# Kernel tuning notes

Hardware: AMD Instinct MI355X
Metric: run time of the kernel (lower is better)

The kernel has to match this reference:

```python
import jax, jax.numpy as jnp
import numpy as np

B, S, D = 4, 4096, 128

def setup_inputs() -> dict:
    key = jax.random.key(0)
    kq, kk, kv = jax.random.split(key, 3)
    q = jax.random.normal(kq, (B, S, D), dtype=jnp.float32)
    k = jax.random.normal(kk, (B, S, D), dtype=jnp.float32)
    v = jax.random.normal(kv, (B, S, D), dtype=jnp.float32)
    return {"q": q, "k": k, "v": v}

def reference(q, k, v):
    d_model = q.shape[-1]
    scale = 1.0 / jnp.sqrt(jnp.asarray(d_model, q.dtype))
    # [B, S, S] scores
    scores = jnp.einsum('bqd,bkd->bqk', q, k) * scale
    s = q.shape[1]
    causal = jnp.tril(jnp.ones((s, s), dtype=bool))
    neg_inf = jnp.asarray(-jnp.inf, scores.dtype)
    scores = jnp.where(causal[None, :, :], scores, neg_inf)
    attn = jax.nn.softmax(scores, axis=-1)
    return jnp.einsum('bqk,bkd->bqd', attn, v)
```

## Files before the change

kernel.cpp:

```cpp
#include <hip/hip_runtime.h>


#define B_   4
#define S_   4096
#define D_   128
#define BN   64
#define NT_  64
#define QT_  32
#define RMAX 4
#define BLOB_SHORTS 16384
#define MASKVAL (-1.0e30f)

typedef __attribute__((ext_vector_type(8))) short bf16x8;
typedef __attribute__((ext_vector_type(4))) float f32x4;
typedef __attribute__((ext_vector_type(16))) float f32x16;

__device__ __forceinline__ short f2bf(float x) {
    unsigned u = __builtin_bit_cast(unsigned, x);
    unsigned r = (u + 0x7fffu + ((u >> 16) & 1u)) >> 16;
    return (short)r;
}
__device__ __forceinline__ float ex2(float x) { return __builtin_amdgcn_exp2f(x); }
__device__ __forceinline__ unsigned pkbf(float lo, float hi) {
    return (unsigned)(unsigned short)f2bf(lo) | ((unsigned)(unsigned short)f2bf(hi) << 16);
}
__device__ __forceinline__ void gl_lds16(const short* g, short* l) {
    __builtin_amdgcn_global_load_lds(
        (const __attribute__((address_space(1))) unsigned int*)g,
        (__attribute__((address_space(3))) unsigned int*)l, 16, 0, 0);
}

__global__ __launch_bounds__(256) void prep(const float* __restrict__ Qg,
                                            const float* __restrict__ Kg,
                                            const float* __restrict__ Vg,
                                            short* __restrict__ Qbf,
                                            short* __restrict__ KV)
{
    __shared__ short vt[64][40];
    const int id  = blockIdx.x;
    const int tid = threadIdx.x;
    const float SC = 0.12751740f;

    if (id < 1024) {
        const int b = id & 3, tile = (id >> 2) & 63, q4 = id >> 8;
        const int n = q4 * 16 + (tid >> 4);
        const int G = tid & 15;
        const size_t rowoff = ((size_t)b * S_ + (size_t)tile * 64 + n) * D_ + G * 8;
        short* blob = KV + (size_t)(b * NT_ + tile) * BLOB_SHORTS;
        {
            float4 a = *reinterpret_cast<const float4*>(Qg + rowoff);
            float4 c = *reinterpret_cast<const float4*>(Qg + rowoff + 4);
            bf16x8 v;
            v[0] = f2bf(a.x * SC); v[1] = f2bf(a.y * SC); v[2] = f2bf(a.z * SC); v[3] = f2bf(a.w * SC);
            v[4] = f2bf(c.x * SC); v[5] = f2bf(c.y * SC); v[6] = f2bf(c.z * SC); v[7] = f2bf(c.w * SC);
            *reinterpret_cast<bf16x8*>(Qbf + rowoff) = v;
        }
        {
            float4 a = *reinterpret_cast<const float4*>(Kg + rowoff);
            float4 c = *reinterpret_cast<const float4*>(Kg + rowoff + 4);
            bf16x8 v;
            v[0] = f2bf(a.x); v[1] = f2bf(a.y); v[2] = f2bf(a.z); v[3] = f2bf(a.w);
            v[4] = f2bf(c.x); v[5] = f2bf(c.y); v[6] = f2bf(c.z); v[7] = f2bf(c.w);
            const int p = (G & 8) | ((G & 7) ^ (n & 7));
            *reinterpret_cast<bf16x8*>(blob + n * 128 + p * 8) = v;
        }
    } else {
        const int u = id - 1024;
        const int b = u & 3, tile = (u >> 2) & 63, dq = u >> 8;
        short* blob = KV + (size_t)(b * NT_ + tile) * BLOB_SHORTS;
        {
            const int n = tid >> 2, c8 = tid & 3;
            const size_t off = ((size_t)b * S_ + (size_t)tile * 64 + n) * D_ + dq * 32 + c8 * 8;
            float4 a = *reinterpret_cast<const float4*>(Vg + off);
            float4 c = *reinterpret_cast<const float4*>(Vg + off + 4);
            bf16x8 v;
            v[0] = f2bf(a.x); v[1] = f2bf(a.y); v[2] = f2bf(a.z); v[3] = f2bf(a.w);
            v[4] = f2bf(c.x); v[5] = f2bf(c.y); v[6] = f2bf(c.z); v[7] = f2bf(c.w);
            *reinterpret_cast<bf16x8*>(&vt[n][c8 * 8]) = v;
        }
        __syncthreads();
        {
            const int dl = tid >> 3, G = tid & 7;
            const int d  = dq * 32 + dl;
            bf16x8 g;
#pragma unroll
            for (int i = 0; i < 8; ++i) g[i] = vt[G * 8 + i][dl];
            const int p = G ^ (d & 7);
            *reinterpret_cast<bf16x8*>(blob + 8192 + d * 64 + p * 8) = g;
        }
    }
}

template<bool SPLIT>
__global__ __launch_bounds__(256, 2) void fa_fwd(const short* __restrict__ Qbf,
                                                 const short* __restrict__ KV,
                                                 float* __restrict__ Og,
                                                 float* __restrict__ Op,
                                                 float* __restrict__ Ml,
                                                 int R)
{
    __shared__ short lkv[2][BLOB_SHORTS];

    const int tid  = threadIdx.x;
    const int wv   = tid >> 6;
    const int lane = tid & 63;
    const int col  = lane & 31;
    const int half = lane >> 5;
    const int c7   = col & 7;

    int batch, t, lo, hi, chunk_id;
    {
        const int id = blockIdx.x;
        batch = id & 3;
        if (SPLIT) {
            int u = id >> 2;
            int tt = u / R;
            int r  = u - tt * R;
            t  = QT_ - 1 - tt;
            const int nk = 2 * t + 2;
            lo = r * nk / R;
            hi = (r + 1) * nk / R;
            chunk_id = (batch * QT_ + t) * R + r;
            if (lo >= hi) return;
        } else {
            t  = QT_ - 1 - (id >> 2);
            lo = 0; hi = 2 * t + 2; chunk_id = 0;
        }
    }

    bf16x8 qf[8];
    {
        const short* qp = Qbf + ((size_t)batch * S_ + (size_t)t * 128 + wv * 32 + col) * D_ + half * 8;
#pragma unroll
        for (int c = 0; c < 8; ++c)
            qf[c] = *reinterpret_cast<const bf16x8*>(qp + c * 16);
    }

    f32x16 acc[4];
#pragma unroll
    for (int i = 0; i < 4; ++i)
#pragma unroll
        for (int r = 0; r < 16; ++r) acc[i][r] = 0.f;
    float mrun = MASKVAL, lrun = 0.f;

    const size_t tilebase = (size_t)batch * NT_ * BLOB_SHORTS;
#define STAGE(KT, BUF) do {                                                   \
        const short* g_ = KV + tilebase + (size_t)(KT) * BLOB_SHORTS + tid * 8;\
        short* l_ = (BUF) + tid * 8;                                          \
        _Pragma("unroll")                                                     \
        for (int c_ = 0; c_ < 8; ++c_)                                        \
            gl_lds16(g_ + c_ * 2048, l_ + c_ * 2048);                         \
    } while (0)

    STAGE(lo, lkv[0]);

    for (int kt = lo; kt < hi; ++kt) {
        const short* cur = lkv[(kt - lo) & 1];
        short* nxt = lkv[(kt - lo + 1) & 1];
        __syncthreads();
        if (kt + 1 < hi) STAGE(kt + 1, nxt);

        const short* lk = cur;
        const short* lv = cur + 8192;

        f32x16 st[2];
#pragma unroll
        for (int i = 0; i < 2; ++i)
#pragma unroll
            for (int r = 0; r < 16; ++r) st[i][r] = 0.f;
#pragma unroll
        for (int c = 0; c < 8; ++c) {
            const int G = 2 * c + half;
            const int p = (G & 8) | ((G & 7) ^ c7);
#pragma unroll
            for (int kt32 = 0; kt32 < 2; ++kt32) {
                const int n = kt32 * 32 + col;
                bf16x8 kf = *reinterpret_cast<const bf16x8*>(lk + n * 128 + p * 8);
                st[kt32] = __builtin_amdgcn_mfma_f32_32x32x16_bf16(kf, qf[c], st[kt32], 0, 0, 0);
            }
        }

        if (kt >= 2 * t) {
            const int kbase = (kt - 2 * t) * 64;
            const int qloc  = wv * 32 + col;
#pragma unroll
            for (int kt32 = 0; kt32 < 2; ++kt32)
#pragma unroll
                for (int r = 0; r < 16; ++r) {
                    const int kl = kt32 * 32 + (r & 3) + 8 * (r >> 2) + 4 * half;
                    if (kbase + kl > qloc) st[kt32][r] = MASKVAL;
                }
        }

        float mx = MASKVAL;
#pragma unroll
        for (int i = 0; i < 2; ++i)
#pragma unroll
            for (int r = 0; r < 16; ++r) mx = fmaxf(mx, st[i][r]);
        mx = fmaxf(mx, __shfl_xor(mx, 32));
        const float mnew = fmaxf(mrun, mx);
        const float al   = ex2(mrun - mnew);
        mrun = mnew;
        float sum = 0.f;
#pragma unroll
        for (int i = 0; i < 2; ++i)
#pragma unroll
            for (int r = 0; r < 16; ++r) {
                float pv = ex2(st[i][r] - mnew);
                st[i][r] = pv;
                sum += pv;
            }
        sum += __shfl_xor(sum, 32);
        lrun = lrun * al + sum;
#pragma unroll
        for (int i = 0; i < 4; ++i)
#pragma unroll
            for (int r = 0; r < 16; ++r) acc[i][r] *= al;

#pragma unroll
        for (int kt32 = 0; kt32 < 2; ++kt32) {
            unsigned pw[4][2];
#pragma unroll
            for (int w = 0; w < 4; ++w) {
                pw[w][0] = pkbf(st[kt32][4 * w],     st[kt32][4 * w + 1]);
                pw[w][1] = pkbf(st[kt32][4 * w + 2], st[kt32][4 * w + 3]);
            }
#pragma unroll
            for (int s1 = 0; s1 < 2; ++s1) {
                unsigned snd0 = pw[2 * s1 + 1 - half][0];
                unsigned snd1 = pw[2 * s1 + 1 - half][1];
                unsigned rcv0 = __shfl_xor((int)snd0, 32);
                unsigned rcv1 = __shfl_xor((int)snd1, 32);
                unsigned own0 = pw[2 * s1 + half][0];
                unsigned own1 = pw[2 * s1 + half][1];
                int4 wi;
                wi.x = (int)(half ? rcv0 : own0);
                wi.y = (int)(half ? rcv1 : own1);
                wi.z = (int)(half ? own0 : rcv0);
                wi.w = (int)(half ? own1 : rcv1);
                bf16x8 pf = __builtin_bit_cast(bf16x8, wi);
                const int step = kt32 * 2 + s1;
                const int G = 2 * step + half;
                const int p = G ^ c7;
#pragma unroll
                for (int dt = 0; dt < 4; ++dt) {
                    const int d = dt * 32 + col;
                    bf16x8 vf = *reinterpret_cast<const bf16x8*>(lv + d * 64 + p * 8);
                    acc[dt] = __builtin_amdgcn_mfma_f32_32x32x16_bf16(vf, pf, acc[dt], 0, 0, 0);
                }
            }
        }
    }
#undef STAGE

    const int qloc = wv * 32 + col;
    if (SPLIT) {
        float* ob = Op + (size_t)chunk_id * (128 * D_) + (size_t)qloc * D_;
#pragma unroll
        for (int dt = 0; dt < 4; ++dt)
#pragma unroll
            for (int g = 0; g < 4; ++g) {
                const int d0 = dt * 32 + 8 * g + 4 * half;
                f32x4 v4 = {acc[dt][4 * g], acc[dt][4 * g + 1], acc[dt][4 * g + 2], acc[dt][4 * g + 3]};
                *reinterpret_cast<f32x4*>(ob + d0) = v4;
            }
        if (half == 0) {
            float* mlb = Ml + (size_t)chunk_id * (128 * 2) + qloc * 2;
            mlb[0] = mrun;
            mlb[1] = lrun;
        }
    } else {
        const float inv = 1.0f / lrun;
        float* og = Og + ((size_t)batch * S_ + (size_t)t * 128 + qloc) * D_;
#pragma unroll
        for (int dt = 0; dt < 4; ++dt)
#pragma unroll
            for (int g = 0; g < 4; ++g) {
                const int d0 = dt * 32 + 8 * g + 4 * half;
                f32x4 v4 = {acc[dt][4 * g] * inv, acc[dt][4 * g + 1] * inv,
                            acc[dt][4 * g + 2] * inv, acc[dt][4 * g + 3] * inv};
                *reinterpret_cast<f32x4*>(og + d0) = v4;
            }
    }
}

template<int RR>
__global__ __launch_bounds__(256) void fa_merge(const float* __restrict__ Op,
                                                const float* __restrict__ Ml,
                                                float* __restrict__ Og)
{
    const int x   = blockIdx.x;
    const int btq = x >> 4;
    const int oct = x & 15;
    const int t   = btq & (QT_ - 1);
    const int nk  = 2 * t + 2;
    const int row = oct * 8 + (threadIdx.x >> 5);
    const int cg  = threadIdx.x & 31;
    const size_t cbase = (size_t)btq * RR;

    float mg = MASKVAL;
#pragma unroll
    for (int r = 0; r < RR; ++r) {
        int lo = r * nk / RR, hi = (r + 1) * nk / RR;
        if (lo < hi) mg = fmaxf(mg, Ml[(cbase + r) * (128 * 2) + row * 2]);
    }
    float l = 0.f;
    f32x4 a = (f32x4){0.f, 0.f, 0.f, 0.f};
#pragma unroll
    for (int r = 0; r < RR; ++r) {
        int lo = r * nk / RR, hi = (r + 1) * nk / RR;
        if (lo >= hi) continue;
        float mr = Ml[(cbase + r) * (128 * 2) + row * 2];
        float lr = Ml[(cbase + r) * (128 * 2) + row * 2 + 1];
        float w  = ex2(mr - mg);
        l += lr * w;
        a += w * *reinterpret_cast<const f32x4*>(Op + (cbase + r) * (128 * D_) + row * D_ + cg * 4);
    }
    *reinterpret_cast<f32x4*>(Og + (size_t)btq * (128 * D_) + row * D_ + cg * 4) = a * (1.0f / l);
}

extern "C" void kernel_launch(void* const* d_in, const int* in_sizes, int n_in,
                              void* d_out, int out_size, void* d_ws, size_t ws_size,
                              hipStream_t stream) {
    const float* q = (const float*)d_in[0];
    const float* k = (const float*)d_in[1];
    const float* v = (const float*)d_in[2];
    float* o = (float*)d_out;

    const size_t QBF_BYTES = (size_t)B_ * S_ * D_ * 2;
    const size_t KV_BYTES  = (size_t)B_ * NT_ * BLOB_SHORTS * 2;
    const size_t PREFIX    = QBF_BYTES + KV_BYTES;
    const size_t O_FLOATS  = (size_t)B_ * QT_ * 128 * D_;
    const size_t ML_FLOATS = (size_t)B_ * QT_ * 128 * 2;
    const size_t PER_R     = (O_FLOATS + ML_FLOATS) * sizeof(float);

    char* ws = (char*)d_ws;
    short* Qbf = (short*)ws;
    short* KV  = (short*)(ws + QBF_BYTES);

    int R = 0;
    if (ws_size > PREFIX) {
        R = (int)((ws_size - PREFIX) / PER_R);
        if (R > RMAX) R = RMAX;
    }

    prep<<<dim3(2048), 256, 0, stream>>>(q, k, v, Qbf, KV);

    if (R >= 1) {
        float* Op = (float*)(ws + PREFIX);
        float* Ml = Op + (size_t)R * O_FLOATS;
        fa_fwd<true><<<dim3(B_ * QT_ * R), 256, 0, stream>>>(Qbf, KV, nullptr, Op, Ml, R);
        switch (R) {
            case 1: fa_merge<1><<<dim3(B_ * QT_ * 16), 256, 0, stream>>>(Op, Ml, o); break;
            case 2: fa_merge<2><<<dim3(B_ * QT_ * 16), 256, 0, stream>>>(Op, Ml, o); break;
            case 3: fa_merge<3><<<dim3(B_ * QT_ * 16), 256, 0, stream>>>(Op, Ml, o); break;
            default: fa_merge<4><<<dim3(B_ * QT_ * 16), 256, 0, stream>>>(Op, Ml, o); break;
        }
    } else {
        fa_fwd<false><<<dim3(B_ * QT_), 256, 0, stream>>>(Qbf, KV, o, nullptr, nullptr, 1);
    }
}
```

Baseline: 124.9 us.

## Replace per-tile KV split with perfectly balanced flattened work partition

Flattens all causal (query tile, KV tile) pairs per batch into one linear sequence of 1056 units and gives each of 128 blocks per batch an equal contiguous slice of about 8 units. Blocks that cross query-tile boundaries flush partial outputs and reload Q, so every block does the same amount of work instead of splitting each query tile into a fixed R chunks. Partial outputs are now stored as bf16 to halve merge traffic. This trades extra partial-slot writes and bf16 rounding of partials for even load across CUs, and the merge kernel now reads a variable number of slots per tile.

```diff
diff --git a/kernel.cpp b/kernel.cpp
--- a/kernel.cpp
+++ b/kernel.cpp
@@ -4,10 +4,11 @@
 #define B_   4
 #define S_   4096
 #define D_   128
-#define BN   64
 #define NT_  64
 #define QT_  32
-#define RMAX 4
+#define JB   128
+#define W_   1056
+#define SLOTS_PB 160
 #define BLOB_SHORTS 16384
 #define MASKVAL (-1.0e30f)
 
@@ -24,11 +25,15 @@
 __device__ __forceinline__ unsigned pkbf(float lo, float hi) {
     return (unsigned)(unsigned short)f2bf(lo) | ((unsigned)(unsigned short)f2bf(hi) << 16);
 }
+__device__ __forceinline__ float bf2f(short s) {
+    return __builtin_bit_cast(float, ((unsigned)(unsigned short)s) << 16);
+}
 __device__ __forceinline__ void gl_lds16(const short* g, short* l) {
     __builtin_amdgcn_global_load_lds(
         (const __attribute__((address_space(1))) unsigned int*)g,
         (__attribute__((address_space(3))) unsigned int*)l, 16, 0, 0);
 }
+__device__ __forceinline__ int chunk_of(int v) { return (4 * v + 3) / 33; }
 
 __global__ __launch_bounds__(256) void prep(const float* __restrict__ Qg,
                                             const float* __restrict__ Kg,
@@ -91,13 +96,10 @@
     }
 }
 
-template<bool SPLIT>
-__global__ __launch_bounds__(256, 2) void fa_fwd(const short* __restrict__ Qbf,
+__global__ __launch_bounds__(256, 2) void fa_bal(const short* __restrict__ Qbf,
                                                  const short* __restrict__ KV,
-                                                 float* __restrict__ Og,
-                                                 float* __restrict__ Op,
-                                                 float* __restrict__ Ml,
-                                                 int R)
+                                                 short* __restrict__ Opb,
+                                                 float* __restrict__ Ml)
 {
     __shared__ short lkv[2][BLOB_SHORTS];
 
@@ -108,40 +110,23 @@
     const int half = lane >> 5;
     const int c7   = col & 7;
 
-    int batch, t, lo, hi, chunk_id;
-    {
-        const int id = blockIdx.x;
-        batch = id & 3;
-        if (SPLIT) {
-            int u = id >> 2;
-            int tt = u / R;
-            int r  = u - tt * R;
-            t  = QT_ - 1 - tt;
-            const int nk = 2 * t + 2;
-            lo = r * nk / R;
-            hi = (r + 1) * nk / R;
-            chunk_id = (batch * QT_ + t) * R + r;
-            if (lo >= hi) return;
-        } else {
-            t  = QT_ - 1 - (id >> 2);
-            lo = 0; hi = 2 * t + 2; chunk_id = 0;
-        }
-    }
-
-    bf16x8 qf[8];
-    {
-        const short* qp = Qbf + ((size_t)batch * S_ + (size_t)t * 128 + wv * 32 + col) * D_ + half * 8;
-#pragma unroll
-        for (int c = 0; c < 8; ++c)
-            qf[c] = *reinterpret_cast<const bf16x8*>(qp + c * 16);
-    }
-
-    f32x16 acc[4];
-#pragma unroll
-    for (int i = 0; i < 4; ++i)
-#pragma unroll
-        for (int r = 0; r < 16; ++r) acc[i][r] = 0.f;
-    float mrun = MASKVAL, lrun = 0.f;
+    const int batch = blockIdx.x & 3;
+    const int j     = blockIdx.x >> 2;
+    const int v0    = (33 * j) >> 2;
+    const int v1    = (33 * (j + 1)) >> 2;
+
+    int t = (int)((sqrtf((float)(4 * v0 + 1)) - 1.0f) * 0.5f);
+    while ((t + 1) * (t + 2) <= v0) ++t;
+    while (t * (t + 1) > v0) --t;
+    int ktl = v0 - t * (t + 1);
+
+    int base = 0;
+    for (int tt = 0; tt < t; ++tt) {
+        int a = chunk_of(tt * (tt + 1));
+        int b2 = chunk_of((tt + 1) * (tt + 2) - 1);
+        base += b2 - a + 1;
+    }
+    int slot = batch * SLOTS_PB + base + (j - chunk_of(t * (t + 1)));
 
     const size_t tilebase = (size_t)batch * NT_ * BLOB_SHORTS;
 #define STAGE(KT, BUF) do {                                                   \
@@ -151,14 +136,35 @@
         for (int c_ = 0; c_ < 8; ++c_)                                        \
             gl_lds16(g_ + c_ * 2048, l_ + c_ * 2048);                         \
     } while (0)
-
-    STAGE(lo, lkv[0]);
-
-    for (int kt = lo; kt < hi; ++kt) {
-        const short* cur = lkv[(kt - lo) & 1];
-        short* nxt = lkv[(kt - lo + 1) & 1];
+#define LOADQ(T) do {                                                         \
+        const short* qp_ = Qbf + ((size_t)batch * S_ + (size_t)(T) * 128      \
+                                  + wv * 32 + col) * D_ + half * 8;           \
+        _Pragma("unroll")                                                     \
+        for (int c_ = 0; c_ < 8; ++c_)                                        \
+            qf[c_] = *reinterpret_cast<const bf16x8*>(qp_ + c_ * 16);         \
+    } while (0)
+
+    bf16x8 qf[8];
+    LOADQ(t);
+
+    f32x16 acc[4];
+#pragma unroll
+    for (int i = 0; i < 4; ++i)
+#pragma unroll
+        for (int r = 0; r < 16; ++r) acc[i][r] = 0.f;
+    float mrun = MASKVAL, lrun = 0.f;
+
+    STAGE(ktl, lkv[0]);
+
+    for (int v = v0; v < v1; ++v) {
+        const short* cur = lkv[(v - v0) & 1];
+        short* nxt = lkv[(v - v0 + 1) & 1];
+
+        int nt = t, nktl = ktl + 1;
+        if (nktl == 2 * t + 2) { nt = t + 1; nktl = 0; }
+
         __syncthreads();
-        if (kt + 1 < hi) STAGE(kt + 1, nxt);
+        if (v + 1 < v1) STAGE(nktl, nxt);
 
         const short* lk = cur;
         const short* lv = cur + 8192;
@@ -180,8 +186,8 @@
             }
         }
 
-        if (kt >= 2 * t) {
-            const int kbase = (kt - 2 * t) * 64;
+        if (ktl >= 2 * t) {
+            const int kbase = (ktl - 2 * t) * 64;
             const int qloc  = wv * 32 + col;
 #pragma unroll
             for (int kt32 = 0; kt32 < 2; ++kt32)
@@ -239,8 +245,7 @@
                 wi.z = (int)(half ? own0 : rcv0);
                 wi.w = (int)(half ? own1 : rcv1);
                 bf16x8 pf = __builtin_bit_cast(bf16x8, wi);
-                const int step = kt32 * 2 + s1;
-                const int G = 2 * step + half;
+                const int G = 2 * (kt32 * 2 + s1) + half;
                 const int p = G ^ c7;
 #pragma unroll
                 for (int dt = 0; dt < 4; ++dt) {
@@ -250,73 +255,230 @@
                 }
             }
         }
+
+        if (nktl == 0 || v + 1 == v1) {
+            short* ob = Opb + (size_t)slot * (128 * D_) + tid * 64;
+#pragma unroll
+            for (int dt = 0; dt < 4; ++dt)
+#pragma unroll
+                for (int g = 0; g < 4; ++g) {
+                    int2 w;
+                    w.x = (int)pkbf(acc[dt][4 * g],     acc[dt][4 * g + 1]);
+                    w.y = (int)pkbf(acc[dt][4 * g + 2], acc[dt][4 * g + 3]);
+                    *reinterpret_cast<int2*>(ob + (dt * 4 + g) * 4) = w;
+                }
+            if (half == 0) {
+                float* mlb = Ml + (size_t)slot * (128 * 2) + (wv * 32 + col) * 2;
+                mlb[0] = mrun;
+                mlb[1] = lrun;
+            }
+            if (v + 1 < v1) {
+                int a = chunk_of(t * (t + 1));
+                int b2 = chunk_of((t + 1) * (t + 2) - 1);
+                base += b2 - a + 1;
+                slot = batch * SLOTS_PB + base + (j - chunk_of(nt * (nt + 1)));
+                LOADQ(nt);
+#pragma unroll
+                for (int i = 0; i < 4; ++i)
+#pragma unroll
+                    for (int r = 0; r < 16; ++r) acc[i][r] = 0.f;
+                mrun = MASKVAL; lrun = 0.f;
+            }
+        }
+        t = nt; ktl = nktl;
     }
 #undef STAGE
-
-    const int qloc = wv * 32 + col;
-    if (SPLIT) {
-        float* ob = Op + (size_t)chunk_id * (128 * D_) + (size_t)qloc * D_;
-#pragma unroll
-        for (int dt = 0; dt < 4; ++dt)
-#pragma unroll
-            for (int g = 0; g < 4; ++g) {
-                const int d0 = dt * 32 + 8 * g + 4 * half;
-                f32x4 v4 = {acc[dt][4 * g], acc[dt][4 * g + 1], acc[dt][4 * g + 2], acc[dt][4 * g + 3]};
-                *reinterpret_cast<f32x4*>(ob + d0) = v4;
-            }
-        if (half == 0) {
-            float* mlb = Ml + (size_t)chunk_id * (128 * 2) + qloc * 2;
-            mlb[0] = mrun;
-            mlb[1] = lrun;
-        }
-    } else {
-        const float inv = 1.0f / lrun;
-        float* og = Og + ((size_t)batch * S_ + (size_t)t * 128 + qloc) * D_;
-#pragma unroll
-        for (int dt = 0; dt < 4; ++dt)
-#pragma unroll
-            for (int g = 0; g < 4; ++g) {
-                const int d0 = dt * 32 + 8 * g + 4 * half;
-                f32x4 v4 = {acc[dt][4 * g] * inv, acc[dt][4 * g + 1] * inv,
-                            acc[dt][4 * g + 2] * inv, acc[dt][4 * g + 3] * inv};
-                *reinterpret_cast<f32x4*>(og + d0) = v4;
-            }
-    }
-}
-
-template<int RR>
-__global__ __launch_bounds__(256) void fa_merge(const float* __restrict__ Op,
+#undef LOADQ
+}
+
+__global__ __launch_bounds__(256) void fa_merge(const short* __restrict__ Opb,
                                                 const float* __restrict__ Ml,
                                                 float* __restrict__ Og)
 {
     const int x   = blockIdx.x;
     const int btq = x >> 4;
     const int oct = x & 15;
+    const int b   = btq >> 5;
     const int t   = btq & (QT_ - 1);
-    const int nk  = 2 * t + 2;
-    const int row = oct * 8 + (threadIdx.x >> 5);
+    const int q   = oct * 8 + (threadIdx.x >> 5);
     const int cg  = threadIdx.x & 31;
-    const size_t cbase = (size_t)btq * RR;
+
+    const int jlo = chunk_of(t * (t + 1));
+    const int jhi = chunk_of((t + 1) * (t + 2) - 1);
+    const int cnt = jhi - jlo + 1;
+    int base = 0;
+    for (int tt = 0; tt < t; ++tt) {
+        int a = chunk_of(tt * (tt + 1));
+        int b2 = chunk_of((tt + 1) * (tt + 2) - 1);
+        base += b2 - a + 1;
+    }
+    const int slot0 = b * SLOTS_PB + base;
+
+    const int t_id  = (q >> 5) * 64 + (cg & 1) * 32 + (q & 31);
+    const int inner = (cg >> 3) * 4 + ((cg >> 1) & 3);
+    const int d0    = (cg >> 3) * 32 + ((cg >> 1) & 3) * 8 + (cg & 1) * 4;
 
     float mg = MASKVAL;
-#pragma unroll
-    for (int r = 0; r < RR; ++r) {
-        int lo = r * nk / RR, hi = (r + 1) * nk / RR;
-        if (lo < hi) mg = fmaxf(mg, Ml[(cbase + r) * (128 * 2) + row * 2]);
-    }
+    for (int r = 0; r < cnt; ++r)
+        mg = fmaxf(mg, Ml[(size_t)(slot0 + r) * (128 * 2) + q * 2]);
     float l = 0.f;
     f32x4 a = (f32x4){0.f, 0.f, 0.f, 0.f};
-#pragma unroll
-    for (int r = 0; r < RR; ++r) {
-        int lo = r * nk / RR, hi = (r + 1) * nk / RR;
-        if (lo >= hi) continue;
-        float mr = Ml[(cbase + r) * (128 * 2) + row * 2];
-        float lr = Ml[(cbase + r) * (128 * 2) + row * 2 + 1];
+    for (int r = 0; r < cnt; ++r) {
+        const size_t sl = (size_t)(slot0 + r);
+        float mr = Ml[sl * (128 * 2) + q * 2];
+        float lr = Ml[sl * (128 * 2) + q * 2 + 1];
         float w  = ex2(mr - mg);
         l += lr * w;
-        a += w * *reinterpret_cast<const f32x4*>(Op + (cbase + r) * (128 * D_) + row * D_ + cg * 4);
-    }
-    *reinterpret_cast<f32x4*>(Og + (size_t)btq * (128 * D_) + row * D_ + cg * 4) = a * (1.0f / l);
+        short4 s = *reinterpret_cast<const short4*>(
+            Opb + sl * (128 * D_) + t_id * 64 + inner * 4);
+        a[0] += w * bf2f(s.x);
+        a[1] += w * bf2f(s.y);
+        a[2] += w * bf2f(s.z);
+        a[3] += w * bf2f(s.w);
+    }
+    *reinterpret_cast<f32x4*>(Og + (size_t)btq * (128 * D_) + q * D_ + d0) = a * (1.0f / l);
+}
+
+__global__ __launch_bounds__(256, 2) void fa_direct(const short* __restrict__ Qbf,
+                                                    const short* __restrict__ KV,
+                                                    float* __restrict__ Og)
+{
+    __shared__ short lkv[2][BLOB_SHORTS];
+    const int tid  = threadIdx.x;
+    const int wv   = tid >> 6;
+    const int lane = tid & 63;
+    const int col  = lane & 31;
+    const int half = lane >> 5;
+    const int c7   = col & 7;
+    const int batch = blockIdx.x & 3;
+    const int t     = QT_ - 1 - (blockIdx.x >> 2);
+    const int hi    = 2 * t + 2;
+
+    bf16x8 qf[8];
+    {
+        const short* qp = Qbf + ((size_t)batch * S_ + (size_t)t * 128 + wv * 32 + col) * D_ + half * 8;
+#pragma unroll
+        for (int c = 0; c < 8; ++c) qf[c] = *reinterpret_cast<const bf16x8*>(qp + c * 16);
+    }
+    f32x16 acc[4];
+#pragma unroll
+    for (int i = 0; i < 4; ++i)
+#pragma unroll
+        for (int r = 0; r < 16; ++r) acc[i][r] = 0.f;
+    float mrun = MASKVAL, lrun = 0.f;
+    const size_t tilebase = (size_t)batch * NT_ * BLOB_SHORTS;
+#define STAGE(KT, BUF) do {                                                   \
+        const short* g_ = KV + tilebase + (size_t)(KT) * BLOB_SHORTS + tid * 8;\
+        short* l_ = (BUF) + tid * 8;                                          \
+        _Pragma("unroll")                                                     \
+        for (int c_ = 0; c_ < 8; ++c_)                                        \
+            gl_lds16(g_ + c_ * 2048, l_ + c_ * 2048);                         \
+    } while (0)
+    STAGE(0, lkv[0]);
+    for (int kt = 0; kt < hi; ++kt) {
+        const short* cur = lkv[kt & 1];
+        short* nxt = lkv[(kt + 1) & 1];
+        __syncthreads();
+        if (kt + 1 < hi) STAGE(kt + 1, nxt);
+        const short* lk = cur;
+        const short* lv = cur + 8192;
+        f32x16 st[2];
+#pragma unroll
+        for (int i = 0; i < 2; ++i)
+#pragma unroll
+            for (int r = 0; r < 16; ++r) st[i][r] = 0.f;
+#pragma unroll
+        for (int c = 0; c < 8; ++c) {
+            const int G = 2 * c + half;
+            const int p = (G & 8) | ((G & 7) ^ c7);
+#pragma unroll
+            for (int kt32 = 0; kt32 < 2; ++kt32) {
+                const int n = kt32 * 32 + col;
+                bf16x8 kf = *reinterpret_cast<const bf16x8*>(lk + n * 128 + p * 8);
+                st[kt32] = __builtin_amdgcn_mfma_f32_32x32x16_bf16(kf, qf[c], st[kt32], 0, 0, 0);
+            }
+        }
+        if (kt >= 2 * t) {
+            const int kbase = (kt - 2 * t) * 64;
+            const int qloc  = wv * 32 + col;
+#pragma unroll
+            for (int kt32 = 0; kt32 < 2; ++kt32)
+#pragma unroll
+                for (int r = 0; r < 16; ++r) {
+                    const int kl = kt32 * 32 + (r & 3) + 8 * (r >> 2) + 4 * half;
+                    if (kbase + kl > qloc) st[kt32][r] = MASKVAL;
+                }
+        }
+        float mx = MASKVAL;
+#pragma unroll
+        for (int i = 0; i < 2; ++i)
+#pragma unroll
+            for (int r = 0; r < 16; ++r) mx = fmaxf(mx, st[i][r]);
+        mx = fmaxf(mx, __shfl_xor(mx, 32));
+        const float mnew = fmaxf(mrun, mx);
+        const float al   = ex2(mrun - mnew);
+        mrun = mnew;
+        float sum = 0.f;
+#pragma unroll
+        for (int i = 0; i < 2; ++i)
+#pragma unroll
+            for (int r = 0; r < 16; ++r) {
+                float pv = ex2(st[i][r] - mnew);
+                st[i][r] = pv;
+                sum += pv;
+            }
+        sum += __shfl_xor(sum, 32);
+        lrun = lrun * al + sum;
+#pragma unroll
+        for (int i = 0; i < 4; ++i)
+#pragma unroll
+            for (int r = 0; r < 16; ++r) acc[i][r] *= al;
+#pragma unroll
+        for (int kt32 = 0; kt32 < 2; ++kt32) {
+            unsigned pw[4][2];
+#pragma unroll
+            for (int w = 0; w < 4; ++w) {
+                pw[w][0] = pkbf(st[kt32][4 * w],     st[kt32][4 * w + 1]);
+                pw[w][1] = pkbf(st[kt32][4 * w + 2], st[kt32][4 * w + 3]);
+            }
+#pragma unroll
+            for (int s1 = 0; s1 < 2; ++s1) {
+                unsigned snd0 = pw[2 * s1 + 1 - half][0];
+                unsigned snd1 = pw[2 * s1 + 1 - half][1];
+                unsigned rcv0 = __shfl_xor((int)snd0, 32);
+                unsigned rcv1 = __shfl_xor((int)snd1, 32);
+                unsigned own0 = pw[2 * s1 + half][0];
+                unsigned own1 = pw[2 * s1 + half][1];
+                int4 wi;
+                wi.x = (int)(half ? rcv0 : own0);
+                wi.y = (int)(half ? rcv1 : own1);
+                wi.z = (int)(half ? own0 : rcv0);
+                wi.w = (int)(half ? own1 : rcv1);
+                bf16x8 pf = __builtin_bit_cast(bf16x8, wi);
+                const int G = 2 * (kt32 * 2 + s1) + half;
+                const int p = G ^ c7;
+#pragma unroll
+                for (int dt = 0; dt < 4; ++dt) {
+                    const int d = dt * 32 + col;
+                    bf16x8 vf = *reinterpret_cast<const bf16x8*>(lv + d * 64 + p * 8);
+                    acc[dt] = __builtin_amdgcn_mfma_f32_32x32x16_bf16(vf, pf, acc[dt], 0, 0, 0);
+                }
+            }
+        }
+    }
+#undef STAGE
+    const int qloc = wv * 32 + col;
+    const float inv = 1.0f / lrun;
+    float* og = Og + ((size_t)batch * S_ + (size_t)t * 128 + qloc) * D_;
+#pragma unroll
+    for (int dt = 0; dt < 4; ++dt)
+#pragma unroll
+        for (int g = 0; g < 4; ++g) {
+            const int d0 = dt * 32 + 8 * g + 4 * half;
+            f32x4 v4 = {acc[dt][4 * g] * inv, acc[dt][4 * g + 1] * inv,
+                        acc[dt][4 * g + 2] * inv, acc[dt][4 * g + 3] * inv};
+            *reinterpret_cast<f32x4*>(og + d0) = v4;
+        }
 }
 
 extern "C" void kernel_launch(void* const* d_in, const int* in_sizes, int n_in,
@@ -329,34 +491,22 @@
 
     const size_t QBF_BYTES = (size_t)B_ * S_ * D_ * 2;
     const size_t KV_BYTES  = (size_t)B_ * NT_ * BLOB_SHORTS * 2;
-    const size_t PREFIX    = QBF_BYTES + KV_BYTES;
-    const size_t O_FLOATS  = (size_t)B_ * QT_ * 128 * D_;
-    const size_t ML_FLOATS = (size_t)B_ * QT_ * 128 * 2;
-    const size_t PER_R     = (O_FLOATS + ML_FLOATS) * sizeof(float);
+    const size_t OP_BYTES  = (size_t)B_ * SLOTS_PB * 128 * D_ * 2;
+    const size_t ML_BYTES  = (size_t)B_ * SLOTS_PB * 128 * 2 * 4;
+    const size_t NEEDED    = QBF_BYTES + KV_BYTES + OP_BYTES + ML_BYTES;
 
     char* ws = (char*)d_ws;
     short* Qbf = (short*)ws;
     short* KV  = (short*)(ws + QBF_BYTES);
 
-    int R = 0;
-    if (ws_size > PREFIX) {
-        R = (int)((ws_size - PREFIX) / PER_R);
-        if (R > RMAX) R = RMAX;
-    }
-
     prep<<<dim3(2048), 256, 0, stream>>>(q, k, v, Qbf, KV);
 
-    if (R >= 1) {
-        float* Op = (float*)(ws + PREFIX);
-        float* Ml = Op + (size_t)R * O_FLOATS;
-        fa_fwd<true><<<dim3(B_ * QT_ * R), 256, 0, stream>>>(Qbf, KV, nullptr, Op, Ml, R);
-        switch (R) {
-            case 1: fa_merge<1><<<dim3(B_ * QT_ * 16), 256, 0, stream>>>(Op, Ml, o); break;
-            case 2: fa_merge<2><<<dim3(B_ * QT_ * 16), 256, 0, stream>>>(Op, Ml, o); break;
-            case 3: fa_merge<3><<<dim3(B_ * QT_ * 16), 256, 0, stream>>>(Op, Ml, o); break;
-            default: fa_merge<4><<<dim3(B_ * QT_ * 16), 256, 0, stream>>>(Op, Ml, o); break;
-        }
+    if (ws_size >= NEEDED) {
+        short* Opb = (short*)(ws + QBF_BYTES + KV_BYTES);
+        float* Ml  = (float*)(ws + QBF_BYTES + KV_BYTES + OP_BYTES);
+        fa_bal<<<dim3(B_ * JB), 256, 0, stream>>>(Qbf, KV, Opb, Ml);
+        fa_merge<<<dim3(B_ * QT_ * 16), 256, 0, stream>>>(Opb, Ml, o);
     } else {
-        fa_fwd<false><<<dim3(B_ * QT_), 256, 0, stream>>>(Qbf, KV, o, nullptr, nullptr, 1);
-    }
-}
+        fa_direct<<<dim3(B_ * QT_), 256, 0, stream>>>(Qbf, KV, o);
+    }
+}
```

Measured after the change: 124.6 us. No clear change (-0.3%).
